# Kernel optimization log

Measured on AMD Instinct MI355X. Metric: run time of the kernel, lower is better.

The kernel has to match this reference:

```python
import jax, jax.numpy as jnp
import numpy as np

NEG = -1000000.0  # mask fill value used by original sequence_mask

def setup_inputs() -> dict:
    key = jax.random.key(0)
    k1, k2, k3, k4 = jax.random.split(key, 4)
    B, S, D = 32, 2048, 64
    queries = jax.random.normal(k1, (B, S, D), dtype=jnp.float32)
    keys = jax.random.normal(k2, (B, S, D), dtype=jnp.float32)
    values = jax.random.normal(k3, (B, S, D), dtype=jnp.float32)
    valid_lens = jax.random.randint(k4, (B,), 1, S + 1, dtype=jnp.int64)
    return {"queries": queries, "keys": keys, "values": values, "valid_lens": valid_lens}

def reference(queries, keys, values, valid_lens):
    d = queries.shape[-1]
    # [B, Sq, Sk]
    scores = jnp.einsum('bqd,bkd->bqk', queries, keys) / jnp.sqrt(jnp.asarray(d, queries.dtype))
    # valid_lens is 1D: one length per batch row, broadcast over all query rows
    kv_idx = jnp.arange(scores.shape[-1])  # [Sk]
    mask = kv_idx[None, None, :] < valid_lens[:, None, None]  # [B,1,Sk] broadcast
    scores = jnp.where(mask, scores, jnp.asarray(NEG, scores.dtype))
    weights = jax.nn.softmax(scores, axis=-1)
    # dropout p=0.0 -> identity
    return jnp.einsum('bqk,bkd->bqd', weights, values)
```

## Files before the change

### kernel.cpp

```cpp
#include <hip/hip_runtime.h>
#include <hip/hip_bf16.h>

typedef __attribute__((ext_vector_type(8))) short bf16x8;
typedef __attribute__((ext_vector_type(4))) float f32x4;

#define BATCH 32
#define SEQ   2048
#define PSTR  20
#define KSTR  72
#define VSTR  36
#define LOG2E 1.44269504088896340736f
#define QSCALE (0.125f * LOG2E)
#define NEGL  (-1000000.0f * LOG2E)

__device__ __forceinline__ unsigned int pk2(float lo, float hi) {
    __hip_bfloat162 h2 = __float22bfloat162_rn(make_float2(lo, hi));
    return *reinterpret_cast<unsigned int*>(&h2);
}

__device__ __forceinline__ void dma16(const short* g, short* l) {
    __builtin_amdgcn_global_load_lds((const __attribute__((address_space(1))) void*)g,
                                     (__attribute__((address_space(3))) void*)l, 16, 0, 0);
}

__global__ void prep_vl(const int* __restrict__ VL, int* __restrict__ meta) {
    __shared__ int sv[BATCH];
    const int t = threadIdx.x;
    int odd = (t < 16) ? VL[2 * t + 1] : 0;
    const bool is64 = (__ballot(odd != 0) == 0ULL);
    if (t < BATCH) {
        int x = is64 ? VL[2 * t] : VL[t];
        x = x < 0 ? 0 : (x > SEQ ? SEQ : x);
        sv[t] = x;
    }
    __syncthreads();
    if (t < BATCH) {
        const int x = sv[t];
        int rank = 0;
        for (int j = 0; j < BATCH; ++j) {
            const int y = sv[j];
            rank += (y > x) || (y == x && j < t);
        }
        meta[rank] = x;
        meta[BATCH + rank] = t;
    }
}

__global__ __launch_bounds__(256) void prepkv(const float* __restrict__ Kp,
                                              const float* __restrict__ Vp,
                                              short* __restrict__ Kb,
                                              short* __restrict__ Vt) {
    __shared__ unsigned int l[64 * VSTR];
    const int tid = threadIdx.x;
    const int b = blockIdx.x >> 5, kt = blockIdx.x & 31, kb = kt * 64;
    const float* Kv = Kp + ((size_t)b * SEQ + kb) * 64;
    const float* Vb = Vp + ((size_t)b * SEQ + kb) * 64;
    #pragma unroll
    for (int h = 0; h < 4; ++h) {
        const int c = tid + h * 256;
        const int row = c >> 4, col = (c & 15) * 4;
        f32x4 x = *(const f32x4*)(Kv + row * 64 + col);
        unsigned int* dst = (unsigned int*)(Kb + ((size_t)b * SEQ + kb + row) * 64 + col);
        dst[0] = pk2(x[0], x[1]); dst[1] = pk2(x[2], x[3]);
    }
    #pragma unroll
    for (int h = 0; h < 2; ++h) {
        const int u = tid + h * 256;
        const int d4 = (u & 3) + ((u >> 7) << 2);
        const int kp = (u >> 2) & 31;
        f32x4 a = *(const f32x4*)(Vb + (2 * kp) * 64 + d4 * 4);
        f32x4 c = *(const f32x4*)(Vb + (2 * kp + 1) * 64 + d4 * 4);
        #pragma unroll
        for (int j = 0; j < 4; ++j)
            l[(d4 * 4 + j) * VSTR + kp] = pk2(a[j], c[j]);
    }
    __syncthreads();
    const int d = tid >> 2, cg = tid & 3;
    unsigned int w[8];
    #pragma unroll
    for (int j = 0; j < 8; ++j) w[j] = l[d * VSTR + cg * 8 + j];
    unsigned int* dst = (unsigned int*)(Vt + (size_t)(b * 64 + d) * SEQ + kb + cg * 16);
    #pragma unroll
    for (int j = 0; j < 8; ++j) dst[j] = w[j];
}

__global__ __launch_bounds__(256, 3)
void attn_fwd(const float* __restrict__ Qp, const short* __restrict__ Kb,
              const short* __restrict__ Vt, const int* __restrict__ meta,
              float* __restrict__ Out) {
    constexpr int S = SEQ;
    constexpr int qtiles = S >> 6;
    __shared__ short bK2[2 * 64 * 64];
    __shared__ short bV2[2 * 64 * 64];
    __shared__ unsigned int lPt[4 * 32 * PSTR];

    const int tid  = threadIdx.x;
    const int wave = tid >> 6, lane = tid & 63;
    const int l15  = lane & 15, grp = lane >> 4;
    const int r7   = l15 & 7;

    const int slot = blockIdx.x / qtiles, qt = blockIdx.x % qtiles;
    const int vl = meta[slot], batch = meta[BATCH + slot];
    const int ntiles = (vl + 63) >> 6;

    const short* Kbb = Kb + (size_t)batch * S * 64;
    const short* Vtb = Vt + (size_t)batch * 64 * S;

    const int r8 = lane >> 3, s8 = lane & 7, csw = s8 ^ r8;
    const short* gK0 = Kbb + (wave * 16 + r8) * 64 + csw * 8;
    const short* gV0 = Vtb + (size_t)(wave * 16 + r8) * S + csw * 8;
    short* lK0 = &bK2[wave * 16 * 64];
    short* lV0 = &bV2[wave * 16 * 64];

    bf16x8 qf[2];
    {
        const float* qb = Qp + ((size_t)batch * S + qt * 64 + wave * 16 + l15) * 64 + grp * 8;
        #pragma unroll
        for (int kf = 0; kf < 2; ++kf) {
            f32x4 a = *(const f32x4*)(qb + kf * 32);
            f32x4 c = *(const f32x4*)(qb + kf * 32 + 4);
            union { bf16x8 v; unsigned int u[4]; } qq;
            qq.u[0] = pk2(a[0] * QSCALE, a[1] * QSCALE);
            qq.u[1] = pk2(a[2] * QSCALE, a[3] * QSCALE);
            qq.u[2] = pk2(c[0] * QSCALE, c[1] * QSCALE);
            qq.u[3] = pk2(c[2] * QSCALE, c[3] * QSCALE);
            qf[kf] = qq.v;
        }
    }

    f32x4 o[4] = {{0.f,0.f,0.f,0.f},{0.f,0.f,0.f,0.f},{0.f,0.f,0.f,0.f},{0.f,0.f,0.f,0.f}};
    float mrun = -INFINITY, lrun = 0.f;
    unsigned int* pw = &lPt[wave * 32 * PSTR];

    if (ntiles > 0) {
        dma16(gK0,                    lK0);
        dma16(gK0 + 8 * 64,           lK0 + 8 * 64);
        dma16(gV0,                    lV0);
        dma16(gV0 + (size_t)8 * S,    lV0 + 8 * 64);
    }

    for (int kt = 0; kt < ntiles; ++kt) {
        __syncthreads();
        if (kt + 1 < ntiles) {
            const int nb  = ((kt + 1) & 1) * 4096;
            const int kbn = (kt + 1) * 64;
            dma16(gK0 + kbn * 64,                  lK0 + nb);
            dma16(gK0 + kbn * 64 + 8 * 64,         lK0 + nb + 8 * 64);
            dma16(gV0 + kbn,                       lV0 + nb);
            dma16(gV0 + kbn + (size_t)8 * S,       lV0 + nb + 8 * 64);
        }
        const short* bK = &bK2[(kt & 1) * 4096];
        const short* bV = &bV2[(kt & 1) * 4096];

        f32x4 st[4] = {{0.f,0.f,0.f,0.f},{0.f,0.f,0.f,0.f},{0.f,0.f,0.f,0.f},{0.f,0.f,0.f,0.f}};
        #pragma unroll
        for (int kf = 0; kf < 2; ++kf) {
            #pragma unroll
            for (int ct = 0; ct < 4; ++ct) {
                bf16x8 kfr = *(const bf16x8*)&bK[((ct * 16 + l15) << 6) +
                                                 (((kf * 4 + grp) ^ r7) << 3)];
                st[ct] = __builtin_amdgcn_mfma_f32_16x16x32_bf16(kfr, qf[kf], st[ct], 0, 0, 0);
            }
        }

        if (kt == ntiles - 1 && (vl & 63) != 0) {
            const int kbase = kt * 64;
            #pragma unroll
            for (int ct = 0; ct < 4; ++ct)
                #pragma unroll
                for (int r = 0; r < 4; ++r) {
                    const bool valid = (kbase + ct * 16 + grp * 4 + r) < vl;
                    st[ct][r] = valid ? st[ct][r] : NEGL;
                }
        }

        float t0 = fmaxf(fmaxf(st[0][0], st[0][1]), fmaxf(st[0][2], st[0][3]));
        float t1 = fmaxf(fmaxf(st[1][0], st[1][1]), fmaxf(st[1][2], st[1][3]));
        float t2 = fmaxf(fmaxf(st[2][0], st[2][1]), fmaxf(st[2][2], st[2][3]));
        float t3 = fmaxf(fmaxf(st[3][0], st[3][1]), fmaxf(st[3][2], st[3][3]));
        float tm = fmaxf(fmaxf(t0, t1), fmaxf(t2, t3));
        tm = fmaxf(tm, __shfl_xor(tm, 16));
        tm = fmaxf(tm, __shfl_xor(tm, 32));
        if (__ballot(tm > mrun) != 0ULL) {
            const float mnew  = fmaxf(mrun, tm);
            const float alpha = exp2f(mrun - mnew);
            mrun = mnew;
            lrun *= alpha;
            #pragma unroll
            for (int dt = 0; dt < 4; ++dt)
                #pragma unroll
                for (int r = 0; r < 4; ++r) o[dt][r] *= alpha;
        }

        float rs = 0.f;
        #pragma unroll
        for (int ct = 0; ct < 4; ++ct) {
            #pragma unroll
            for (int r = 0; r < 4; ++r) {
                st[ct][r] = exp2f(st[ct][r] - mrun);
                rs += st[ct][r];
            }
            #pragma unroll
            for (int a = 0; a < 2; ++a)
                pw[(ct * 8 + grp * 2 + a) * PSTR + l15] = pk2(st[ct][2 * a], st[ct][2 * a + 1]);
        }
        rs += __shfl_xor(rs, 16);
        rs += __shfl_xor(rs, 32);
        lrun += rs;
        asm volatile("s_waitcnt lgkmcnt(0)" ::: "memory");

        #pragma unroll
        for (int kk = 0; kk < 2; ++kk) {
            union { bf16x8 v; unsigned int u[4]; } pf;
            #pragma unroll
            for (int jj = 0; jj < 4; ++jj)
                pf.u[jj] = pw[(kk * 16 + grp * 4 + jj) * PSTR + l15];
            #pragma unroll
            for (int dt = 0; dt < 4; ++dt) {
                bf16x8 vf = *(const bf16x8*)&bV[((dt * 16 + l15) << 6) +
                                                (((kk * 4 + grp) ^ r7) << 3)];
                o[dt] = __builtin_amdgcn_mfma_f32_16x16x32_bf16(vf, pf.v, o[dt], 0, 0, 0);
            }
        }
    }

    const float inv = (lrun > 0.f) ? 1.0f / lrun : 0.f;
    const size_t orow = ((size_t)batch * S + qt * 64 + wave * 16 + l15) * 64;
    #pragma unroll
    for (int dt = 0; dt < 4; ++dt) {
        f32x4 w = o[dt];
        w[0] *= inv; w[1] *= inv; w[2] *= inv; w[3] *= inv;
        *(f32x4*)(Out + orow + dt * 16 + grp * 4) = w;
    }
}

__device__ __forceinline__ void load_tile_fb(const float* __restrict__ Kb,
                                             const float* __restrict__ Vb,
                                             int tid, f32x4 kv[4], f32x4 vv[4]) {
    #pragma unroll
    for (int h = 0; h < 4; ++h) {
        const int c = tid + h * 256;
        kv[h] = *(const f32x4*)(Kb + (c >> 4) * 64 + (c & 15) * 4);
    }
    #pragma unroll
    for (int h = 0; h < 2; ++h) {
        const int u  = tid + h * 256;
        const int d4 = (u & 3) + ((u >> 7) << 2);
        const int kp = (u >> 2) & 31;
        vv[2 * h]     = *(const f32x4*)(Vb + (2 * kp) * 64 + d4 * 4);
        vv[2 * h + 1] = *(const f32x4*)(Vb + (2 * kp + 1) * 64 + d4 * 4);
    }
}

__global__ __launch_bounds__(256, 4)
void attn_fb(const float* __restrict__ Qp, const float* __restrict__ Kp,
             const float* __restrict__ Vp, const int* __restrict__ meta,
             float* __restrict__ Out) {
    constexpr int S = SEQ;
    constexpr int qtiles = S >> 6;
    __shared__ short        lK [64 * KSTR];
    __shared__ unsigned int lVt[64 * VSTR];
    __shared__ unsigned int lPt[4 * 32 * PSTR];
    const int tid = threadIdx.x;
    const int wave = tid >> 6, lane = tid & 63;
    const int l15 = lane & 15, grp = lane >> 4;
    const int slot = blockIdx.x / qtiles, qt = blockIdx.x % qtiles;
    const int vl = meta[slot], batch = meta[BATCH + slot];
    const int ntiles = (vl + 63) >> 6;
    const float* Kb = Kp + (size_t)batch * S * 64;
    const float* Vb = Vp + (size_t)batch * S * 64;
    bf16x8 qf[2];
    {
        const float* qb = Qp + ((size_t)batch * S + qt * 64 + wave * 16 + l15) * 64 + grp * 8;
        #pragma unroll
        for (int kf = 0; kf < 2; ++kf) {
            f32x4 a = *(const f32x4*)(qb + kf * 32);
            f32x4 b = *(const f32x4*)(qb + kf * 32 + 4);
            union { bf16x8 v; unsigned int u[4]; } qq;
            qq.u[0] = pk2(a[0], a[1]); qq.u[1] = pk2(a[2], a[3]);
            qq.u[2] = pk2(b[0], b[1]); qq.u[3] = pk2(b[2], b[3]);
            qf[kf] = qq.v;
        }
    }
    f32x4 o[4] = {{0.f,0.f,0.f,0.f},{0.f,0.f,0.f,0.f},{0.f,0.f,0.f,0.f},{0.f,0.f,0.f,0.f}};
    float mrun = -INFINITY, lrun = 0.f;
    unsigned int* pw = &lPt[wave * 32 * PSTR];
    f32x4 kv[4], vv[4];
    if (ntiles > 0) load_tile_fb(Kb, Vb, tid, kv, vv);
    for (int kt = 0; kt < ntiles; ++kt) {
        const int kb = kt * 64;
        __syncthreads();
        #pragma unroll
        for (int h = 0; h < 4; ++h) {
            const int c = tid + h * 256;
            const int row = c >> 4, col = (c & 15) * 4;
            union { f32x4 f; float e[4]; } x; x.f = kv[h];
            unsigned int* dst = (unsigned int*)&lK[row * KSTR + col];
            dst[0] = pk2(x.e[0], x.e[1]); dst[1] = pk2(x.e[2], x.e[3]);
        }
        #pragma unroll
        for (int h = 0; h < 2; ++h) {
            const int u  = tid + h * 256;
            const int d4 = (u & 3) + ((u >> 7) << 2);
            const int kp = (u >> 2) & 31;
            union { f32x4 f; float e[4]; } a, b;
            a.f = vv[2 * h]; b.f = vv[2 * h + 1];
            #pragma unroll
            for (int j = 0; j < 4; ++j)
                lVt[(d4 * 4 + j) * VSTR + kp] = pk2(a.e[j], b.e[j]);
        }
        if (kt + 1 < ntiles) load_tile_fb(Kb + (size_t)(kb + 64) * 64, Vb + (size_t)(kb + 64) * 64, tid, kv, vv);
        __syncthreads();
        f32x4 st[4] = {{0.f,0.f,0.f,0.f},{0.f,0.f,0.f,0.f},{0.f,0.f,0.f,0.f},{0.f,0.f,0.f,0.f}};
        #pragma unroll
        for (int kf = 0; kf < 2; ++kf) {
            #pragma unroll
            for (int ct = 0; ct < 4; ++ct) {
                bf16x8 kfr = *(const bf16x8*)&lK[(ct * 16 + l15) * KSTR + kf * 32 + grp * 8];
                st[ct] = __builtin_amdgcn_mfma_f32_16x16x32_bf16(kfr, qf[kf], st[ct], 0, 0, 0);
            }
        }
        #pragma unroll
        for (int ct = 0; ct < 4; ++ct)
            #pragma unroll
            for (int r = 0; r < 4; ++r) {
                const bool valid = (kb + ct * 16 + grp * 4 + r) < vl;
                st[ct][r] = valid ? st[ct][r] * (0.125f * LOG2E) : NEGL;
            }
        float t0 = fmaxf(fmaxf(st[0][0], st[0][1]), fmaxf(st[0][2], st[0][3]));
        float t1 = fmaxf(fmaxf(st[1][0], st[1][1]), fmaxf(st[1][2], st[1][3]));
        float t2 = fmaxf(fmaxf(st[2][0], st[2][1]), fmaxf(st[2][2], st[2][3]));
        float t3 = fmaxf(fmaxf(st[3][0], st[3][1]), fmaxf(st[3][2], st[3][3]));
        float tm = fmaxf(fmaxf(t0, t1), fmaxf(t2, t3));
        tm = fmaxf(tm, __shfl_xor(tm, 16));
        tm = fmaxf(tm, __shfl_xor(tm, 32));
        const float mnew  = fmaxf(mrun, tm);
        const float alpha = exp2f(mrun - mnew);
        mrun = mnew;
        lrun *= alpha;
        #pragma unroll
        for (int dt = 0; dt < 4; ++dt)
            #pragma unroll
            for (int r = 0; r < 4; ++r) o[dt][r] *= alpha;
        float rs = 0.f;
        #pragma unroll
        for (int ct = 0; ct < 4; ++ct) {
            #pragma unroll
            for (int r = 0; r < 4; ++r) {
                st[ct][r] = exp2f(st[ct][r] - mrun);
                rs += st[ct][r];
            }
            #pragma unroll
            for (int a = 0; a < 2; ++a)
                pw[(ct * 8 + grp * 2 + a) * PSTR + l15] = pk2(st[ct][2 * a], st[ct][2 * a + 1]);
        }
        rs += __shfl_xor(rs, 16);
        rs += __shfl_xor(rs, 32);
        lrun += rs;
        asm volatile("s_waitcnt lgkmcnt(0)" ::: "memory");
        #pragma unroll
        for (int kk = 0; kk < 2; ++kk) {
            union { bf16x8 v; unsigned int u[4]; } pf;
            #pragma unroll
            for (int jj = 0; jj < 4; ++jj)
                pf.u[jj] = pw[(kk * 16 + grp * 4 + jj) * PSTR + l15];
            #pragma unroll
            for (int dt = 0; dt < 4; ++dt) {
                bf16x8 vf = *(const bf16x8*)&lVt[(dt * 16 + l15) * VSTR + kk * 16 + grp * 4];
                o[dt] = __builtin_amdgcn_mfma_f32_16x16x32_bf16(vf, pf.v, o[dt], 0, 0, 0);
            }
        }
    }
    const float inv = (lrun > 0.f) ? 1.0f / lrun : 0.f;
    const size_t orow = ((size_t)batch * S + qt * 64 + wave * 16 + l15) * 64;
    #pragma unroll
    for (int dt = 0; dt < 4; ++dt) {
        f32x4 w = o[dt];
        w[0] *= inv; w[1] *= inv; w[2] *= inv; w[3] *= inv;
        *(f32x4*)(Out + orow + dt * 16 + grp * 4) = w;
    }
}

extern "C" void kernel_launch(void* const* d_in, const int* in_sizes, int n_in,
                              void* d_out, int out_size, void* d_ws, size_t ws_size,
                              hipStream_t stream) {
    const float* Q  = (const float*)d_in[0];
    const float* K  = (const float*)d_in[1];
    const float* V  = (const float*)d_in[2];
    const int*   VL = (const int*)d_in[3];
    int* meta = (int*)d_ws;
    prep_vl<<<1, 64, 0, stream>>>(VL, meta);
    const size_t need = 256 + 2 * (size_t)BATCH * SEQ * 64 * sizeof(short);
    dim3 grid(BATCH * (SEQ >> 6)), block(256);
    if (ws_size >= need) {
        short* Kb = (short*)((char*)d_ws + 256);
        short* Vt = Kb + (size_t)BATCH * SEQ * 64;
        prepkv<<<dim3(BATCH * 32), block, 0, stream>>>(K, V, Kb, Vt);
        attn_fwd<<<grid, block, 0, stream>>>(Q, Kb, Vt, meta, (float*)d_out);
    } else {
        attn_fb<<<grid, block, 0, stream>>>(Q, K, V, meta, (float*)d_out);
    }
}
```

Before: 141.9 us.

## Fold valid-length prep into prepkv, swizzle P scratch layout, raise occupancy

Removes the separate prep_vl kernel launch in the main path by running the valid-length sort in one extra block of prepkv. It also replaces the padded-stride P scratch layout in LDS with an XOR-style swizzled slot mapping, which shrinks the per-wave buffer and is meant to avoid bank conflicts. It raises the launch-bounds occupancy hint for attn_fwd from 3 to 4 blocks per SM. The higher occupancy target may force register spills, and the swizzle changes LDS access patterns in ways that are hard to predict.

```diff
diff --git a/kernel.cpp b/kernel.cpp
--- a/kernel.cpp
+++ b/kernel.cpp
@@ -21,6 +21,11 @@
 __device__ __forceinline__ void dma16(const short* g, short* l) {
     __builtin_amdgcn_global_load_lds((const __attribute__((address_space(1))) void*)g,
                                      (__attribute__((address_space(3))) void*)l, 16, 0, 0);
+}
+
+__device__ __forceinline__ int pslot(int kp, int q) {
+    const int kp2 = (kp & 0x1A) | ((kp & 1) << 2) | ((kp >> 2) & 1);
+    return (kp2 << 4) + q;
 }
 
 __global__ void prep_vl(const int* __restrict__ VL, int* __restrict__ meta) {
@@ -48,10 +53,36 @@
 
 __global__ __launch_bounds__(256) void prepkv(const float* __restrict__ Kp,
                                               const float* __restrict__ Vp,
+                                              const int* __restrict__ VL,
                                               short* __restrict__ Kb,
-                                              short* __restrict__ Vt) {
+                                              short* __restrict__ Vt,
+                                              int* __restrict__ meta) {
     __shared__ unsigned int l[64 * VSTR];
+    __shared__ int sv[BATCH];
     const int tid = threadIdx.x;
+    if (blockIdx.x == BATCH * 32) {
+        if (tid < 64) {
+            int odd = (tid < 16) ? VL[2 * tid + 1] : 0;
+            const bool is64 = (__ballot(odd != 0) == 0ULL);
+            if (tid < BATCH) {
+                int x = is64 ? VL[2 * tid] : VL[tid];
+                x = x < 0 ? 0 : (x > SEQ ? SEQ : x);
+                sv[tid] = x;
+            }
+            asm volatile("s_waitcnt lgkmcnt(0)" ::: "memory");
+            if (tid < BATCH) {
+                const int x = sv[tid];
+                int rank = 0;
+                for (int j = 0; j < BATCH; ++j) {
+                    const int y = sv[j];
+                    rank += (y > x) || (y == x && j < tid);
+                }
+                meta[rank] = x;
+                meta[BATCH + rank] = tid;
+            }
+        }
+        return;
+    }
     const int b = blockIdx.x >> 5, kt = blockIdx.x & 31, kb = kt * 64;
     const float* Kv = Kp + ((size_t)b * SEQ + kb) * 64;
     const float* Vb = Vp + ((size_t)b * SEQ + kb) * 64;
@@ -84,7 +115,7 @@
     for (int j = 0; j < 8; ++j) dst[j] = w[j];
 }
 
-__global__ __launch_bounds__(256, 3)
+__global__ __launch_bounds__(256, 4)
 void attn_fwd(const float* __restrict__ Qp, const short* __restrict__ Kb,
               const short* __restrict__ Vt, const int* __restrict__ meta,
               float* __restrict__ Out) {
@@ -92,7 +123,7 @@
     constexpr int qtiles = S >> 6;
     __shared__ short bK2[2 * 64 * 64];
     __shared__ short bV2[2 * 64 * 64];
-    __shared__ unsigned int lPt[4 * 32 * PSTR];
+    __shared__ unsigned int lPt[4 * 512];
 
     const int tid  = threadIdx.x;
     const int wave = tid >> 6, lane = tid & 63;
@@ -130,13 +161,13 @@
 
     f32x4 o[4] = {{0.f,0.f,0.f,0.f},{0.f,0.f,0.f,0.f},{0.f,0.f,0.f,0.f},{0.f,0.f,0.f,0.f}};
     float mrun = -INFINITY, lrun = 0.f;
-    unsigned int* pw = &lPt[wave * 32 * PSTR];
+    unsigned int* pw = &lPt[wave * 512];
 
     if (ntiles > 0) {
-        dma16(gK0,                    lK0);
-        dma16(gK0 + 8 * 64,           lK0 + 8 * 64);
-        dma16(gV0,                    lV0);
-        dma16(gV0 + (size_t)8 * S,    lV0 + 8 * 64);
+        dma16(gK0,                 lK0);
+        dma16(gK0 + 8 * 64,        lK0 + 8 * 64);
+        dma16(gV0,                 lV0);
+        dma16(gV0 + (size_t)8 * S, lV0 + 8 * 64);
     }
 
     for (int kt = 0; kt < ntiles; ++kt) {
@@ -144,10 +175,10 @@
         if (kt + 1 < ntiles) {
             const int nb  = ((kt + 1) & 1) * 4096;
             const int kbn = (kt + 1) * 64;
-            dma16(gK0 + kbn * 64,                  lK0 + nb);
-            dma16(gK0 + kbn * 64 + 8 * 64,         lK0 + nb + 8 * 64);
-            dma16(gV0 + kbn,                       lV0 + nb);
-            dma16(gV0 + kbn + (size_t)8 * S,       lV0 + nb + 8 * 64);
+            dma16(gK0 + kbn * 64,            lK0 + nb);
+            dma16(gK0 + kbn * 64 + 8 * 64,   lK0 + nb + 8 * 64);
+            dma16(gV0 + kbn,                 lV0 + nb);
+            dma16(gV0 + kbn + (size_t)8 * S, lV0 + nb + 8 * 64);
         }
         const short* bK = &bK2[(kt & 1) * 4096];
         const short* bV = &bV2[(kt & 1) * 4096];
@@ -202,7 +233,7 @@
             }
             #pragma unroll
             for (int a = 0; a < 2; ++a)
-                pw[(ct * 8 + grp * 2 + a) * PSTR + l15] = pk2(st[ct][2 * a], st[ct][2 * a + 1]);
+                pw[pslot(ct * 8 + grp * 2 + a, l15)] = pk2(st[ct][2 * a], st[ct][2 * a + 1]);
         }
         rs += __shfl_xor(rs, 16);
         rs += __shfl_xor(rs, 32);
@@ -214,7 +245,7 @@
             union { bf16x8 v; unsigned int u[4]; } pf;
             #pragma unroll
             for (int jj = 0; jj < 4; ++jj)
-                pf.u[jj] = pw[(kk * 16 + grp * 4 + jj) * PSTR + l15];
+                pf.u[jj] = pw[pslot(kk * 16 + grp * 4 + jj, l15)];
             #pragma unroll
             for (int dt = 0; dt < 4; ++dt) {
                 bf16x8 vf = *(const bf16x8*)&bV[((dt * 16 + l15) << 6) +
@@ -389,15 +420,15 @@
     const float* V  = (const float*)d_in[2];
     const int*   VL = (const int*)d_in[3];
     int* meta = (int*)d_ws;
-    prep_vl<<<1, 64, 0, stream>>>(VL, meta);
     const size_t need = 256 + 2 * (size_t)BATCH * SEQ * 64 * sizeof(short);
     dim3 grid(BATCH * (SEQ >> 6)), block(256);
     if (ws_size >= need) {
         short* Kb = (short*)((char*)d_ws + 256);
         short* Vt = Kb + (size_t)BATCH * SEQ * 64;
-        prepkv<<<dim3(BATCH * 32), block, 0, stream>>>(K, V, Kb, Vt);
+        prepkv<<<dim3(BATCH * 32 + 1), block, 0, stream>>>(K, V, VL, Kb, Vt, meta);
         attn_fwd<<<grid, block, 0, stream>>>(Q, Kb, Vt, meta, (float*)d_out);
     } else {
+        prep_vl<<<1, 64, 0, stream>>>(VL, meta);
         attn_fb<<<grid, block, 0, stream>>>(Q, K, V, meta, (float*)d_out);
     }
 }
```

Result: no change. 141.0 us (-0.6%).
